# Optimization experiments

Hardware: AMD Instinct MI355X
Metric: run time of the kernel (lower is better)

Reference implementation:

```python
import jax, jax.numpy as jnp
import numpy as np

CODEBOOK_SIZE = 1024
EMBEDDING_DIM = 64


def setup_inputs() -> dict:
    key = jax.random.key(0)
    k_in, k_cb = jax.random.split(key)
    # latent feature (batch, embedding_dim, length)
    input = jax.random.normal(k_in, (16, EMBEDDING_DIM, 8192), dtype=jnp.float32)
    # learned codebook table (codebook_size, embedding_dim)
    codebook = jax.random.normal(k_cb, (CODEBOOK_SIZE, EMBEDDING_DIM), dtype=jnp.float32)
    return {"input": input, "codebook": codebook}


def reference(input, codebook):
    # input: (B, D, T); codebook: (K, D)
    B, D = input.shape[0], input.shape[1]
    spatial = input.shape[2:]
    # move embedding dim last and flatten tokens: (B*T, D)
    x = jnp.moveaxis(input, 1, -1).reshape(-1, D)
    x_sq = jnp.sum(x * x, axis=-1, keepdims=True)            # (N, 1)
    e_sq = jnp.sum(codebook * codebook, axis=-1)             # (K,)
    dist = x_sq - 2.0 * (x @ codebook.T) + e_sq[None, :]     # (N, K)
    indices = jnp.argmin(dist, axis=-1)                      # (N,)
    quantized = jnp.take(codebook, indices, axis=0)          # (N, D)
    # reshape back: output (B, D, *spatial), indices (B, *spatial)
    out = jnp.moveaxis(quantized.reshape((B,) + spatial + (D,)), -1, 1)
    idx = indices.reshape((B,) + spatial)
    return out, idx
```

## Files before the change

kernel.cpp:

```cpp
#include <hip/hip_runtime.h>
#include <float.h>

#define K_CODES 1024
#define DIM 64
#define T_LEN 8192
#define N_TOK 131072
#define LO_SCALE 2048.0f

typedef _Float16 half8 __attribute__((ext_vector_type(8)));
typedef float    f32x4 __attribute__((ext_vector_type(4)));

#define MFMA16(a, b, c) __builtin_amdgcn_mfma_f32_16x16x32_f16((a), (b), (c), 0, 0, 0)

__global__ void vq_prep(const float* __restrict__ cb,
                        _Float16* __restrict__ w,
                        float* __restrict__ wesq) {
    __shared__ float part[128];
    const int ct   = blockIdx.x;
    const int r    = threadIdx.x;
    const int halF = r >> 7;
    const int rr   = r & 127;
    const int q    = rr >> 4;
    const int code = rr & 15;

    const float* src = cb + (size_t)(ct * 16 + code) * DIM + q * 8;
    float4 v0 = *reinterpret_cast<const float4*>(src);
    float4 v1 = *reinterpret_cast<const float4*>(src + 4);
    float x[8] = {v0.x, v0.y, v0.z, v0.w, v1.x, v1.y, v1.z, v1.w};

    half8 o;
    float psum = 0.0f;
    #pragma unroll
    for (int j = 0; j < 8; ++j) {
        _Float16 h = (_Float16)x[j];
        o[j] = halF ? (_Float16)((x[j] - (float)h) * LO_SCALE) : h;
        psum = fmaf(x[j], x[j], psum);
    }
    *reinterpret_cast<half8*>(w + (size_t)ct * 2048 + halF * 1024 + q * 128 + code * 8) = o;

    if (halF == 0) part[rr] = psum;
    __syncthreads();
    if (r < 16) {
        float s = 0.0f;
        #pragma unroll
        for (int q2 = 0; q2 < 8; ++q2) s += part[q2 * 16 + r];
        wesq[ct * 16 + r] = s * LO_SCALE;
    }
}

__global__ __launch_bounds__(256, 2)
void vq_main(const float* __restrict__ in,
             const float* __restrict__ cb,
             const _Float16* __restrict__ w,
             const float* __restrict__ wesq,
             float* __restrict__ out) {
    __shared__ float esq_s[K_CODES];
    __shared__ int   idx_s[256];

    const int tid  = threadIdx.x;
    const int wave = tid >> 6;
    const int lane = tid & 63;
    const int lo4  = lane & 15;
    const int quad = lane >> 4;

    for (int k = tid; k < K_CODES; k += 256) esq_s[k] = wesq[k];
    __syncthreads();

    const int strip = blockIdx.x * 256 + wave * 64;
    const int b  = strip >> 13;
    const int t0 = strip & 8191;

    const float* xin = in + (size_t)b * DIM * T_LEN + t0;
    half8 a_h[4][2], a_hs[4][2], a_l[4][2];
    #pragma unroll
    for (int mt = 0; mt < 4; ++mt) {
        #pragma unroll
        for (int s = 0; s < 2; ++s) {
            half8 hh, hs, ll;
            #pragma unroll
            for (int j = 0; j < 8; ++j) {
                const int d = s * 32 + quad * 8 + j;
                float xv = -2.0f * xin[(size_t)d * T_LEN + mt * 16 + lo4];
                _Float16 h = (_Float16)xv;
                hh[j] = h;
                hs[j] = (_Float16)((float)h * LO_SCALE);
                ll[j] = (_Float16)((xv - (float)h) * LO_SCALE);
            }
            a_h[mt][s] = hh;
            a_hs[mt][s] = hs;
            a_l[mt][s] = ll;
        }
    }

    float best[16];
    int   bidx[16];
    #pragma unroll
    for (int i = 0; i < 16; ++i) { best[i] = FLT_MAX; bidx[i] = 0; }

    const _Float16* wb = w + (size_t)lane * 8;

    half8 Ah0, Ah1, Al0, Al1, Bh0, Bh1, Bl0, Bl1;
    float Ae, Be;
    auto loadB = [&](int ct, half8& h0, half8& h1, half8& l0, half8& l1, float& es) {
        const _Float16* p = wb + (size_t)ct * 2048;
        h0 = *reinterpret_cast<const half8*>(p);
        h1 = *reinterpret_cast<const half8*>(p + 512);
        l0 = *reinterpret_cast<const half8*>(p + 1024);
        l1 = *reinterpret_cast<const half8*>(p + 1536);
        es = esq_s[ct * 16 + lo4];
    };
    auto step = [&](const half8& h0, const half8& h1, const half8& l0,
                    const half8& l1, float es, int ct) {
        const int code = ct * 16 + lo4;
        #pragma unroll
        for (int mt = 0; mt < 4; ++mt) {
            f32x4 c = {es, es, es, es};
            c = MFMA16(a_hs[mt][0], h0, c);
            c = MFMA16(a_hs[mt][1], h1, c);
            c = MFMA16(a_h[mt][0], l0, c);
            c = MFMA16(a_h[mt][1], l1, c);
            c = MFMA16(a_l[mt][0], h0, c);
            c = MFMA16(a_l[mt][1], h1, c);
            #pragma unroll
            for (int r = 0; r < 4; ++r) {
                float sc = c[r];
                const int i = mt * 4 + r;
                bool lt = sc < best[i];
                best[i] = lt ? sc : best[i];
                bidx[i] = lt ? code : bidx[i];
            }
        }
    };

    loadB(0, Ah0, Ah1, Al0, Al1, Ae);
    loadB(1, Bh0, Bh1, Bl0, Bl1, Be);
    for (int p = 0; p < 31; ++p) {
        step(Ah0, Ah1, Al0, Al1, Ae, 2 * p);
        loadB(2 * p + 2, Ah0, Ah1, Al0, Al1, Ae);
        step(Bh0, Bh1, Bl0, Bl1, Be, 2 * p + 1);
        loadB(2 * p + 3, Bh0, Bh1, Bl0, Bl1, Be);
    }
    step(Ah0, Ah1, Al0, Al1, Ae, 62);
    step(Bh0, Bh1, Bl0, Bl1, Be, 63);

    #pragma unroll
    for (int i = 0; i < 16; ++i) {
        float s = best[i];
        int  ix = bidx[i];
        #pragma unroll
        for (int off = 1; off < 16; off <<= 1) {
            float s2 = __shfl_xor(s, off, 64);
            int  ix2 = __shfl_xor(ix, off, 64);
            bool take = (s2 < s) || (s2 == s && ix2 < ix);
            s  = take ? s2 : s;
            ix = take ? ix2 : ix;
        }
        if (lo4 == 0) {
            idx_s[wave * 64 + (i >> 2) * 16 + quad * 4 + (i & 3)] = ix;
        }
    }
    __syncthreads();

    const int token = blockIdx.x * 256 + tid;
    const int tb = token >> 13;
    const int tt = token & 8191;
    const int my_idx = idx_s[tid];

    out[(size_t)N_TOK * DIM + token] = (float)my_idx;

    const float* crow = cb + (size_t)my_idx * DIM;
    float* outv = out + (size_t)tb * DIM * T_LEN + tt;
    #pragma unroll
    for (int d0 = 0; d0 < DIM; d0 += 4) {
        float4 v = *reinterpret_cast<const float4*>(crow + d0);
        outv[(size_t)(d0 + 0) * T_LEN] = v.x;
        outv[(size_t)(d0 + 1) * T_LEN] = v.y;
        outv[(size_t)(d0 + 2) * T_LEN] = v.z;
        outv[(size_t)(d0 + 3) * T_LEN] = v.w;
    }
}

extern "C" void kernel_launch(void* const* d_in, const int* in_sizes, int n_in,
                              void* d_out, int out_size, void* d_ws, size_t ws_size,
                              hipStream_t stream) {
    const float* in = (const float*)d_in[0];
    const float* cb = (const float*)d_in[1];
    float* out = (float*)d_out;

    _Float16* w   = (_Float16*)d_ws;
    float*   wesq = (float*)((char*)d_ws + 64 * 4096);

    vq_prep<<<dim3(64), dim3(256), 0, stream>>>(cb, w, wesq);
    vq_main<<<dim3(N_TOK / 256), dim3(256), 0, stream>>>(in, cb, w, wesq, out);
}
```

Baseline: 128.2 us.

## Switch distance GEMM to 32x32x16 MFMA tiles with prescaled codebook halves

Replaces the 16x16x32 f16 MFMA tiling with 32x32x16 MFMAs, reorganising codebook staging into 32-code tiles and the token operand into 2 row tiles of 32. The LO_SCALE factor moves onto the codebook side so the token operand needs only hi and lo halves, dropping one prescaled register copy. Larger MFMA tiles raise operand reuse per instruction. The trade-off is a larger 16-register accumulator, doubled best/index arrays and a longer 5-step shuffle reduction, which add register pressure.

```diff
diff --git a/kernel.cpp b/kernel.cpp
--- a/kernel.cpp
+++ b/kernel.cpp
@@ -7,44 +7,47 @@
 #define N_TOK 131072
 #define LO_SCALE 2048.0f
 
-typedef _Float16 half8 __attribute__((ext_vector_type(8)));
-typedef float    f32x4 __attribute__((ext_vector_type(4)));
-
-#define MFMA16(a, b, c) __builtin_amdgcn_mfma_f32_16x16x32_f16((a), (b), (c), 0, 0, 0)
+typedef _Float16 half8  __attribute__((ext_vector_type(8)));
+typedef float    f32x16 __attribute__((ext_vector_type(16)));
+
+#define MFMA32(a, b, c) __builtin_amdgcn_mfma_f32_32x32x16_f16((a), (b), (c), 0, 0, 0)
 
 __global__ void vq_prep(const float* __restrict__ cb,
                         _Float16* __restrict__ w,
                         float* __restrict__ wesq) {
-    __shared__ float part[128];
+    __shared__ float part[256];
     const int ct   = blockIdx.x;
-    const int r    = threadIdx.x;
-    const int halF = r >> 7;
-    const int rr   = r & 127;
-    const int q    = rr >> 4;
-    const int code = rr & 15;
-
-    const float* src = cb + (size_t)(ct * 16 + code) * DIM + q * 8;
+    const int t    = threadIdx.x;
+    const int kc   = t >> 6;
+    const int lane = t & 63;
+    const int n    = lane & 31;
+    const int kh   = lane >> 5;
+
+    const float* src = cb + (size_t)(ct * 32 + n) * DIM + kc * 16 + kh * 8;
     float4 v0 = *reinterpret_cast<const float4*>(src);
     float4 v1 = *reinterpret_cast<const float4*>(src + 4);
     float x[8] = {v0.x, v0.y, v0.z, v0.w, v1.x, v1.y, v1.z, v1.w};
 
-    half8 o;
+    half8 hs, ls;
     float psum = 0.0f;
     #pragma unroll
     for (int j = 0; j < 8; ++j) {
-        _Float16 h = (_Float16)x[j];
-        o[j] = halF ? (_Float16)((x[j] - (float)h) * LO_SCALE) : h;
+        _Float16 bh = (_Float16)x[j];
+        hs[j] = (_Float16)((float)bh * LO_SCALE);
+        ls[j] = (_Float16)((x[j] - (float)bh) * LO_SCALE);
         psum = fmaf(x[j], x[j], psum);
     }
-    *reinterpret_cast<half8*>(w + (size_t)ct * 2048 + halF * 1024 + q * 128 + code * 8) = o;
-
-    if (halF == 0) part[rr] = psum;
+    _Float16* wt = w + (size_t)ct * 4096;
+    *reinterpret_cast<half8*>(wt + 0 * 2048 + kc * 512 + lane * 8) = hs;
+    *reinterpret_cast<half8*>(wt + 1 * 2048 + kc * 512 + lane * 8) = ls;
+
+    part[t] = psum;
     __syncthreads();
-    if (r < 16) {
+    if (t < 32) {
         float s = 0.0f;
         #pragma unroll
-        for (int q2 = 0; q2 < 8; ++q2) s += part[q2 * 16 + r];
-        wesq[ct * 16 + r] = s * LO_SCALE;
+        for (int g = 0; g < 8; ++g) s += part[g * 32 + t];
+        wesq[ct * 32 + t] = s * LO_SCALE;
     }
 }
 
@@ -60,8 +63,8 @@
     const int tid  = threadIdx.x;
     const int wave = tid >> 6;
     const int lane = tid & 63;
-    const int lo4  = lane & 15;
-    const int quad = lane >> 4;
+    const int n5   = lane & 31;
+    const int kh   = lane >> 5;
 
     for (int k = tid; k < K_CODES; k += 256) esq_s[k] = wesq[k];
     __syncthreads();
@@ -71,60 +74,60 @@
     const int t0 = strip & 8191;
 
     const float* xin = in + (size_t)b * DIM * T_LEN + t0;
-    half8 a_h[4][2], a_hs[4][2], a_l[4][2];
-    #pragma unroll
-    for (int mt = 0; mt < 4; ++mt) {
-        #pragma unroll
-        for (int s = 0; s < 2; ++s) {
-            half8 hh, hs, ll;
+    half8 a_h[2][4], a_l[2][4];
+    #pragma unroll
+    for (int mt = 0; mt < 2; ++mt) {
+        #pragma unroll
+        for (int kc = 0; kc < 4; ++kc) {
+            half8 hh, ll;
             #pragma unroll
             for (int j = 0; j < 8; ++j) {
-                const int d = s * 32 + quad * 8 + j;
-                float xv = -2.0f * xin[(size_t)d * T_LEN + mt * 16 + lo4];
-                _Float16 h = (_Float16)xv;
-                hh[j] = h;
-                hs[j] = (_Float16)((float)h * LO_SCALE);
-                ll[j] = (_Float16)((xv - (float)h) * LO_SCALE);
+                const int d = kc * 16 + kh * 8 + j;
+                float xv = -2.0f * xin[(size_t)d * T_LEN + mt * 32 + n5];
+                _Float16 ah = (_Float16)xv;
+                hh[j] = ah;
+                ll[j] = (_Float16)(xv - (float)ah);
             }
-            a_h[mt][s] = hh;
-            a_hs[mt][s] = hs;
-            a_l[mt][s] = ll;
-        }
-    }
-
-    float best[16];
-    int   bidx[16];
-    #pragma unroll
-    for (int i = 0; i < 16; ++i) { best[i] = FLT_MAX; bidx[i] = 0; }
+            a_h[mt][kc] = hh;
+            a_l[mt][kc] = ll;
+        }
+    }
+
+    float best[32];
+    int   bidx[32];
+    #pragma unroll
+    for (int i = 0; i < 32; ++i) { best[i] = FLT_MAX; bidx[i] = 0; }
 
     const _Float16* wb = w + (size_t)lane * 8;
 
-    half8 Ah0, Ah1, Al0, Al1, Bh0, Bh1, Bl0, Bl1;
+    half8 Ah[4], Al[4], Bh[4], Bl[4];
     float Ae, Be;
-    auto loadB = [&](int ct, half8& h0, half8& h1, half8& l0, half8& l1, float& es) {
-        const _Float16* p = wb + (size_t)ct * 2048;
-        h0 = *reinterpret_cast<const half8*>(p);
-        h1 = *reinterpret_cast<const half8*>(p + 512);
-        l0 = *reinterpret_cast<const half8*>(p + 1024);
-        l1 = *reinterpret_cast<const half8*>(p + 1536);
-        es = esq_s[ct * 16 + lo4];
+    auto loadB = [&](int ct, half8* h, half8* l, float& es) {
+        const _Float16* p = wb + (size_t)ct * 4096;
+        #pragma unroll
+        for (int kc = 0; kc < 4; ++kc) {
+            h[kc] = *reinterpret_cast<const half8*>(p + kc * 512);
+            l[kc] = *reinterpret_cast<const half8*>(p + 2048 + kc * 512);
+        }
+        es = esq_s[ct * 32 + n5];
     };
-    auto step = [&](const half8& h0, const half8& h1, const half8& l0,
-                    const half8& l1, float es, int ct) {
-        const int code = ct * 16 + lo4;
-        #pragma unroll
-        for (int mt = 0; mt < 4; ++mt) {
-            f32x4 c = {es, es, es, es};
-            c = MFMA16(a_hs[mt][0], h0, c);
-            c = MFMA16(a_hs[mt][1], h1, c);
-            c = MFMA16(a_h[mt][0], l0, c);
-            c = MFMA16(a_h[mt][1], l1, c);
-            c = MFMA16(a_l[mt][0], h0, c);
-            c = MFMA16(a_l[mt][1], h1, c);
-            #pragma unroll
-            for (int r = 0; r < 4; ++r) {
+    auto step = [&](const half8* h, const half8* l, float es, int ct) {
+        const int code = ct * 32 + n5;
+        #pragma unroll
+        for (int mt = 0; mt < 2; ++mt) {
+            f32x16 c;
+            #pragma unroll
+            for (int r = 0; r < 16; ++r) c[r] = es;
+            #pragma unroll
+            for (int kc = 0; kc < 4; ++kc) c = MFMA32(a_h[mt][kc], h[kc], c);
+            #pragma unroll
+            for (int kc = 0; kc < 4; ++kc) c = MFMA32(a_h[mt][kc], l[kc], c);
+            #pragma unroll
+            for (int kc = 0; kc < 4; ++kc) c = MFMA32(a_l[mt][kc], h[kc], c);
+            #pragma unroll
+            for (int r = 0; r < 16; ++r) {
                 float sc = c[r];
-                const int i = mt * 4 + r;
+                const int i = mt * 16 + r;
                 bool lt = sc < best[i];
                 best[i] = lt ? sc : best[i];
                 bidx[i] = lt ? code : bidx[i];
@@ -132,31 +135,33 @@
         }
     };
 
-    loadB(0, Ah0, Ah1, Al0, Al1, Ae);
-    loadB(1, Bh0, Bh1, Bl0, Bl1, Be);
-    for (int p = 0; p < 31; ++p) {
-        step(Ah0, Ah1, Al0, Al1, Ae, 2 * p);
-        loadB(2 * p + 2, Ah0, Ah1, Al0, Al1, Ae);
-        step(Bh0, Bh1, Bl0, Bl1, Be, 2 * p + 1);
-        loadB(2 * p + 3, Bh0, Bh1, Bl0, Bl1, Be);
-    }
-    step(Ah0, Ah1, Al0, Al1, Ae, 62);
-    step(Bh0, Bh1, Bl0, Bl1, Be, 63);
-
-    #pragma unroll
-    for (int i = 0; i < 16; ++i) {
+    loadB(0, Ah, Al, Ae);
+    loadB(1, Bh, Bl, Be);
+    for (int p = 0; p < 15; ++p) {
+        step(Ah, Al, Ae, 2 * p);
+        loadB(2 * p + 2, Ah, Al, Ae);
+        step(Bh, Bl, Be, 2 * p + 1);
+        loadB(2 * p + 3, Bh, Bl, Be);
+    }
+    step(Ah, Al, Ae, 30);
+    step(Bh, Bl, Be, 31);
+
+    #pragma unroll
+    for (int i = 0; i < 32; ++i) {
         float s = best[i];
         int  ix = bidx[i];
         #pragma unroll
-        for (int off = 1; off < 16; off <<= 1) {
+        for (int off = 1; off < 32; off <<= 1) {
             float s2 = __shfl_xor(s, off, 64);
             int  ix2 = __shfl_xor(ix, off, 64);
             bool take = (s2 < s) || (s2 == s && ix2 < ix);
             s  = take ? s2 : s;
             ix = take ? ix2 : ix;
         }
-        if (lo4 == 0) {
-            idx_s[wave * 64 + (i >> 2) * 16 + quad * 4 + (i & 3)] = ix;
+        if (n5 == 0) {
+            const int mt = i >> 4, r = i & 15;
+            const int row = (r & 3) + 8 * (r >> 2) + 4 * kh;
+            idx_s[wave * 64 + mt * 32 + row] = ix;
         }
     }
     __syncthreads();
@@ -188,8 +193,8 @@
     float* out = (float*)d_out;
 
     _Float16* w   = (_Float16*)d_ws;
-    float*   wesq = (float*)((char*)d_ws + 64 * 4096);
-
-    vq_prep<<<dim3(64), dim3(256), 0, stream>>>(cb, w, wesq);
+    float*   wesq = (float*)((char*)d_ws + 32 * 8192);
+
+    vq_prep<<<dim3(32), dim3(256), 0, stream>>>(cb, w, wesq);
     vq_main<<<dim3(N_TOK / 256), dim3(256), 0, stream>>>(in, cb, w, wesq, out);
 }
```

Measured after the change: 140.6 us. 9.7% more time.

## Split codebook search across wave pairs and raise occupancy to four blocks

Applied to the files above, without the earlier changes.

Each block now covers 128 tokens instead of 256. Two waves share each 64-token strip, and each of the pair scans half of the codebook (512 codes), so the serial loop length per wave is halved. Partial minima are merged through shared memory with an extra barrier. The output gather is split across two thread halves by embedding dimension. Launch bounds rise to 4 blocks per CU, which caps registers per thread and risks spills given the large A-fragment and best/index arrays. The A-operand conversion work per token is duplicated across the wave pair.

```diff
diff --git a/kernel.cpp b/kernel.cpp
--- a/kernel.cpp
+++ b/kernel.cpp
@@ -48,25 +48,29 @@
     }
 }
 
-__global__ __launch_bounds__(256, 2)
+__global__ __launch_bounds__(256, 4)
 void vq_main(const float* __restrict__ in,
              const float* __restrict__ cb,
              const _Float16* __restrict__ w,
              const float* __restrict__ wesq,
              float* __restrict__ out) {
     __shared__ float esq_s[K_CODES];
-    __shared__ int   idx_s[256];
-
-    const int tid  = threadIdx.x;
-    const int wave = tid >> 6;
-    const int lane = tid & 63;
-    const int lo4  = lane & 15;
-    const int quad = lane >> 4;
+    __shared__ float kbest[2][128];
+    __shared__ int   kidx[2][128];
+    __shared__ int   idx_s[128];
+
+    const int tid   = threadIdx.x;
+    const int wave  = tid >> 6;
+    const int lane  = tid & 63;
+    const int lo4   = lane & 15;
+    const int quad  = lane >> 4;
+    const int sid   = wave & 1;
+    const int khalf = wave >> 1;
 
     for (int k = tid; k < K_CODES; k += 256) esq_s[k] = wesq[k];
     __syncthreads();
 
-    const int strip = blockIdx.x * 256 + wave * 64;
+    const int strip = blockIdx.x * 128 + sid * 64;
     const int b  = strip >> 13;
     const int t0 = strip & 8191;
 
@@ -97,7 +101,8 @@
     #pragma unroll
     for (int i = 0; i < 16; ++i) { best[i] = FLT_MAX; bidx[i] = 0; }
 
-    const _Float16* wb = w + (size_t)lane * 8;
+    const _Float16* wb = w + (size_t)khalf * 32 * 2048 + (size_t)lane * 8;
+    const int code0 = khalf * 512;
 
     half8 Ah0, Ah1, Al0, Al1, Bh0, Bh1, Bl0, Bl1;
     float Ae, Be;
@@ -107,11 +112,11 @@
         h1 = *reinterpret_cast<const half8*>(p + 512);
         l0 = *reinterpret_cast<const half8*>(p + 1024);
         l1 = *reinterpret_cast<const half8*>(p + 1536);
-        es = esq_s[ct * 16 + lo4];
+        es = esq_s[code0 + ct * 16 + lo4];
     };
     auto step = [&](const half8& h0, const half8& h1, const half8& l0,
                     const half8& l1, float es, int ct) {
-        const int code = ct * 16 + lo4;
+        const int code = code0 + ct * 16 + lo4;
         #pragma unroll
         for (int mt = 0; mt < 4; ++mt) {
             f32x4 c = {es, es, es, es};
@@ -134,14 +139,14 @@
 
     loadB(0, Ah0, Ah1, Al0, Al1, Ae);
     loadB(1, Bh0, Bh1, Bl0, Bl1, Be);
-    for (int p = 0; p < 31; ++p) {
+    for (int p = 0; p < 15; ++p) {
         step(Ah0, Ah1, Al0, Al1, Ae, 2 * p);
         loadB(2 * p + 2, Ah0, Ah1, Al0, Al1, Ae);
         step(Bh0, Bh1, Bl0, Bl1, Be, 2 * p + 1);
         loadB(2 * p + 3, Bh0, Bh1, Bl0, Bl1, Be);
     }
-    step(Ah0, Ah1, Al0, Al1, Ae, 62);
-    step(Bh0, Bh1, Bl0, Bl1, Be, 63);
+    step(Ah0, Ah1, Al0, Al1, Ae, 30);
+    step(Bh0, Bh1, Bl0, Bl1, Be, 31);
 
     #pragma unroll
     for (int i = 0; i < 16; ++i) {
@@ -156,22 +161,33 @@
             ix = take ? ix2 : ix;
         }
         if (lo4 == 0) {
-            idx_s[wave * 64 + (i >> 2) * 16 + quad * 4 + (i & 3)] = ix;
-        }
-    }
-    __syncthreads();
-
-    const int token = blockIdx.x * 256 + tid;
+            const int tl = (i >> 2) * 16 + quad * 4 + (i & 3);
+            kbest[khalf][sid * 64 + tl] = s;
+            kidx [khalf][sid * 64 + tl] = ix;
+        }
+    }
+    __syncthreads();
+
+    if (tid < 128) {
+        float s0 = kbest[0][tid], s1 = kbest[1][tid];
+        idx_s[tid] = (s1 < s0) ? kidx[1][tid] : kidx[0][tid];
+    }
+    __syncthreads();
+
+    const int tok_local = tid & 127;
+    const int dhalf = tid >> 7;
+    const int token = blockIdx.x * 128 + tok_local;
     const int tb = token >> 13;
     const int tt = token & 8191;
-    const int my_idx = idx_s[tid];
-
-    out[(size_t)N_TOK * DIM + token] = (float)my_idx;
-
-    const float* crow = cb + (size_t)my_idx * DIM;
-    float* outv = out + (size_t)tb * DIM * T_LEN + tt;
-    #pragma unroll
-    for (int d0 = 0; d0 < DIM; d0 += 4) {
+    const int my_idx = idx_s[tok_local];
+
+    if (dhalf == 0)
+        out[(size_t)N_TOK * DIM + token] = (float)my_idx;
+
+    const float* crow = cb + (size_t)my_idx * DIM + dhalf * 32;
+    float* outv = out + (size_t)tb * DIM * T_LEN + (size_t)(dhalf * 32) * T_LEN + tt;
+    #pragma unroll
+    for (int d0 = 0; d0 < 32; d0 += 4) {
         float4 v = *reinterpret_cast<const float4*>(crow + d0);
         outv[(size_t)(d0 + 0) * T_LEN] = v.x;
         outv[(size_t)(d0 + 1) * T_LEN] = v.y;
@@ -191,5 +207,5 @@
     float*   wesq = (float*)((char*)d_ws + 64 * 4096);
 
     vq_prep<<<dim3(64), dim3(256), 0, stream>>>(cb, w, wesq);
-    vq_main<<<dim3(N_TOK / 256), dim3(256), 0, stream>>>(in, cb, w, wesq, out);
+    vq_main<<<dim3(N_TOK / 128), dim3(256), 0, stream>>>(in, cb, w, wesq, out);
 }
```

Result: slower. 473.3 us (+269.3%).
